# Performance work log

Measured on AMD Instinct MI355X. Metric: run time of the kernel, lower is better.

The kernel has to match this reference:

```python
import jax, jax.numpy as jnp
import numpy as np

TEMPERATURE = 0.1
B, T, D = 8, 1024, 1024
NEG_INF = -1e30

def setup_inputs() -> dict:
    key = jax.random.key(0)
    k1, k2, k3 = jax.random.split(key, 3)
    features = jax.random.normal(k1, (B, T, D), dtype=jnp.float32)
    masks = jax.random.bernoulli(k2, 0.05, (B, 1, T, T)).astype(jnp.float32)
    input_coords_length = jax.random.randint(k3, (B,), T // 2, T - 1)  # int32
    return {"features": features, "masks": masks, "input_coords_length": input_coords_length}


def _sup_con_loss(feat, mask, L):
    # feat: [T, D], mask: [T, T] float, L: scalar int valid length (slice [:L, :L])
    Tn = feat.shape[0]
    dt = feat.dtype
    vr = jnp.arange(Tn) < L                              # valid rows/cols [T]
    valid2d = (vr[:, None] & vr[None, :]).astype(dt)     # [T, T]
    dot = jnp.matmul(feat, feat.T) / TEMPERATURE         # [T, T]
    dot = jnp.where(vr[None, :], dot, NEG_INF)           # exclude padded cols from max
    logits = dot - jax.lax.stop_gradient(jnp.max(dot, axis=-1, keepdims=True))
    logits_mask = (1.0 - jnp.eye(Tn, dtype=dt)) * valid2d  # off-diagonal, in-slice
    exp_logits = jnp.exp(logits) * logits_mask
    m = mask * valid2d
    # negative_mask = 1-mask; entries < 1 zeroed (binary mask -> indicator of mask==0)
    neg = 1.0 - m
    neg = jnp.where(neg < 1.0, 0.0, neg) * valid2d
    # positive_mask = mask with entries > 0 set to 1
    pos = jnp.where(m > 0, 1.0, m)
    neg_denom = jnp.sum(exp_logits * neg, axis=-1, keepdims=True)
    pos_denom = jax.lax.stop_gradient(jnp.sum(exp_logits * pos, axis=-1, keepdims=True))
    log_prob = logits - jnp.log(neg_denom + pos_denom + 1e-6)
    m2 = m * logits_mask
    mean_log_prob_pos = (m2 * log_prob).sum(-1) / (m2.sum(-1) + 1e-6)  # [T]
    # mean over the L valid rows only (matches .mean() on the sliced tensor)
    return -jnp.sum(jnp.where(vr, mean_log_prob_pos, 0.0)) / L.astype(dt)


def _is_valid(mask, L):
    # valid sample iff sliced mask differs from eye(L) with [0,0]=0
    Tn = mask.shape[0]
    vr = jnp.arange(Tn) < L
    valid2d = (vr[:, None] & vr[None, :]).astype(mask.dtype)
    sanity = jnp.eye(Tn, dtype=mask.dtype).at[0, 0].set(0.0) * valid2d
    return jnp.any((mask * valid2d) != sanity)


def reference(features, masks, input_coords_length):
    L = input_coords_length + 1                      # [B]
    mask0 = masks[:, 0]                              # [B, T, T] (num_layers asserted == 1)
    losses = jax.vmap(_sup_con_loss)(features, mask0, L)   # [B]
    valid = jax.vmap(_is_valid)(mask0, L)                  # [B] bool
    vbs = jnp.maximum(jnp.sum(valid.astype(features.dtype)), 1.0)
    return jnp.sum(losses) / vbs
```

## Files before the change

kernel.cpp:

```cpp
#include <hip/hip_runtime.h>
#include <hip/hip_bf16.h>
#include <stdint.h>

#define T_DIM 1024
#define B_DIM 8

typedef __attribute__((ext_vector_type(8))) short short8;
typedef __attribute__((ext_vector_type(4))) float f32x4;

__device__ inline void gll16(const void* g, void* l) {
  __builtin_amdgcn_global_load_lds((__attribute__((address_space(1))) void*)g,
                                   (__attribute__((address_space(3))) void*)l,
                                   16, 0, 0);
}

__global__ __launch_bounds__(256) void convert_kernel(const float* __restrict__ F,
                                                      __hip_bfloat16* __restrict__ Fb) {
  const int t = blockIdx.x * 256 + threadIdx.x;
  const float4 v = ((const float4*)F)[t];
  union { __hip_bfloat16 h[4]; uint64_t u; } p;
  p.h[0] = __float2bfloat16(v.x);
  p.h[1] = __float2bfloat16(v.y);
  p.h[2] = __float2bfloat16(v.z);
  p.h[3] = __float2bfloat16(v.w);
  ((uint64_t*)Fb)[t] = p.u;
}

__global__ __launch_bounds__(256) void gram_kernel(const __hip_bfloat16* __restrict__ Fb,
                                                   float* __restrict__ S) {
  __shared__ __hip_bfloat16 As[128 * 32];
  __shared__ __hip_bfloat16 Bs[128 * 32];
  const int b = blockIdx.z;
  const __hip_bfloat16* F = Fb + ((size_t)b << 20);
  float* Sb = S + ((size_t)b << 20);
  const int tid  = threadIdx.x;
  const int lane = tid & 63;
  const int wave = tid >> 6;
  const int wrow = (wave >> 1) * 64;
  const int wcol = (wave & 1) * 64;
  const int row0 = blockIdx.y * 128;
  const int col0 = blockIdx.x * 128;

  const int sr = tid >> 2;
  const int sk = (tid & 3) * 8;

  f32x4 acc[4][4];
#pragma unroll
  for (int i = 0; i < 4; i++)
#pragma unroll
    for (int j = 0; j < 4; j++) acc[i][j] = (f32x4){0.f, 0.f, 0.f, 0.f};

  const int fr = lane & 15;
  const int fk = (lane >> 4) * 8;

  for (int k0 = 0; k0 < T_DIM; k0 += 32) {
    __syncthreads();
    gll16(F + (size_t)(row0 + sr) * T_DIM + k0 + sk,      As + tid * 8);
    gll16(F + (size_t)(row0 + sr + 64) * T_DIM + k0 + sk, As + 64 * 32 + tid * 8);
    gll16(F + (size_t)(col0 + sr) * T_DIM + k0 + sk,      Bs + tid * 8);
    gll16(F + (size_t)(col0 + sr + 64) * T_DIM + k0 + sk, Bs + 64 * 32 + tid * 8);
    __syncthreads();

    short8 af[4], bf[4];
#pragma unroll
    for (int t = 0; t < 4; t++) {
      af[t] = *(const short8*)(As + (wrow + t * 16 + fr) * 32 + fk);
      bf[t] = *(const short8*)(Bs + (wcol + t * 16 + fr) * 32 + fk);
    }
#pragma unroll
    for (int ti = 0; ti < 4; ti++)
#pragma unroll
      for (int tj = 0; tj < 4; tj++)
        acc[ti][tj] = __builtin_amdgcn_mfma_f32_16x16x32_bf16(af[ti], bf[tj], acc[ti][tj], 0, 0, 0);
  }

#pragma unroll
  for (int ti = 0; ti < 4; ti++)
#pragma unroll
    for (int tj = 0; tj < 4; tj++)
#pragma unroll
      for (int r = 0; r < 4; r++) {
        const int row = row0 + wrow + ti * 16 + (lane >> 4) * 4 + r;
        const int col = col0 + wcol + tj * 16 + (lane & 15);
        Sb[(size_t)row * T_DIM + col] = acc[ti][tj][r] * 10.0f;
      }
}

__global__ __launch_bounds__(256) void row_kernel(const float* __restrict__ S,
                                                  const float* __restrict__ M,
                                                  const int* __restrict__ icl,
                                                  float* __restrict__ row_val,
                                                  int* __restrict__ row_bad) {
  const int row = blockIdx.x;
  const int b = row >> 10;
  const int i = row & 1023;
  const int L = icl[b] + 1;
  if (i >= L) {
    if (threadIdx.x == 0) { row_val[row] = 0.0f; row_bad[row] = 0; }
    return;
  }
  const int tid  = threadIdx.x;
  const int lane = tid & 63;
  const int wave = tid >> 6;
  const float4 s4 = ((const float4*)(S + (size_t)row * T_DIM))[tid];
  const float4 m4 = ((const float4*)(M + (size_t)row * T_DIM))[tid];
  const float sv[4] = {s4.x, s4.y, s4.z, s4.w};
  const float mv[4] = {m4.x, m4.y, m4.z, m4.w};
  const int j0 = tid * 4;

  float mx = -1e30f;
#pragma unroll
  for (int c = 0; c < 4; c++)
    if (j0 + c < L) mx = fmaxf(mx, sv[c]);
  for (int o = 32; o > 0; o >>= 1) mx = fmaxf(mx, __shfl_down(mx, o, 64));
  __shared__ float wred[4];
  if (lane == 0) wred[wave] = mx;
  __syncthreads();
  mx = fmaxf(fmaxf(wred[0], wred[1]), fmaxf(wred[2], wred[3]));

  float den = 0.f, cnt = 0.f, asum = 0.f;
  bool bad = false;
#pragma unroll
  for (int c = 0; c < 4; c++) {
    const int j = j0 + c;
    if (j < L) {
      const float d = sv[c] - mx;
      const float mm = mv[c];
      if (j != i) {
        den += __expf(d);
        cnt += mm;
        asum += mm * d;
      }
      const float sane = (j == i && i != 0) ? 1.0f : 0.0f;
      bad = bad || (mm != sane);
    }
  }
  for (int o = 32; o > 0; o >>= 1) {
    den  += __shfl_down(den, o, 64);
    cnt  += __shfl_down(cnt, o, 64);
    asum += __shfl_down(asum, o, 64);
  }
  const bool wbad = (__ballot(bad) != 0ull);
  __shared__ float dred[4], cred[4], ared[4];
  __shared__ int bred[4];
  if (lane == 0) { dred[wave] = den; cred[wave] = cnt; ared[wave] = asum; bred[wave] = wbad ? 1 : 0; }
  __syncthreads();
  if (tid == 0) {
    const float D = dred[0] + dred[1] + dred[2] + dred[3];
    const float C = cred[0] + cred[1] + cred[2] + cred[3];
    const float A = ared[0] + ared[1] + ared[2] + ared[3];
    const float mlpp = (A - C * __logf(D + 1e-6f)) / (C + 1e-6f);
    row_val[row] = -mlpp / (float)L;
    row_bad[row] = bred[0] | bred[1] | bred[2] | bred[3];
  }
}

__global__ __launch_bounds__(256) void final_kernel(const float* __restrict__ row_val,
                                                    const int* __restrict__ row_bad,
                                                    float* __restrict__ out) {
  const int tid  = threadIdx.x;
  const int lane = tid & 63;
  const int wave = tid >> 6;
  __shared__ int vb[B_DIM];
  if (tid < B_DIM) vb[tid] = 0;
  __syncthreads();
  float lsum = 0.f;
  for (int idx = tid; idx < B_DIM * T_DIM; idx += 256) {
    lsum += row_val[idx];
    if (row_bad[idx]) atomicOr(&vb[idx >> 10], 1);
  }
  for (int o = 32; o > 0; o >>= 1) lsum += __shfl_down(lsum, o, 64);
  __shared__ float part[4];
  if (lane == 0) part[wave] = lsum;
  __syncthreads();
  if (tid == 0) {
    const float total = part[0] + part[1] + part[2] + part[3];
    int v = 0;
    for (int b = 0; b < B_DIM; b++) v += (vb[b] ? 1 : 0);
    out[0] = total / fmaxf((float)v, 1.0f);
  }
}

extern "C" void kernel_launch(void* const* d_in, const int* in_sizes, int n_in,
                              void* d_out, int out_size, void* d_ws, size_t ws_size,
                              hipStream_t stream) {
  const float* feat = (const float*)d_in[0];
  const float* mask = (const float*)d_in[1];
  const int*   icl  = (const int*)d_in[2];
  float* out = (float*)d_out;

  char* ws = (char*)d_ws;
  __hip_bfloat16* Fb = (__hip_bfloat16*)ws;
  float* S        = (float*)(ws + (16u << 20));
  float* row_val  = (float*)(ws + (48u << 20));
  int*   row_bad  = (int*)(ws + (48u << 20) + (32u << 10));

  convert_kernel<<<dim3(8192), dim3(256), 0, stream>>>(feat, Fb);
  gram_kernel<<<dim3(8, 8, 8), dim3(256), 0, stream>>>(Fb, S);
  row_kernel<<<dim3(8192), dim3(256), 0, stream>>>(S, mask, icl, row_val, row_bad);
  final_kernel<<<dim3(1), dim3(256), 0, stream>>>(row_val, row_bad, out);
}
```

Measured before the change: 144.0 us.

## Fuse Gram matmul with per-tile online softmax row statistics and skip padded tiles

Replaces the separate Gram-matrix write plus row-reduction kernel with a fused kernel. Each 128x128 tile computes the similarity block and immediately reduces it to per-row partial statistics (running max, exp-sum, masked sum, count, bad flag), merged by a small reduce kernel. This removes the 32MB fp32 S round trip. It also skips tiles entirely past the valid length, loads the operand once for diagonal tiles, and double-buffers 64-wide K stages. In exchange the kernel reads the mask with strided scalar loads in the epilogue and adds more shared memory and register pressure.

```diff
diff --git a/kernel.cpp b/kernel.cpp
--- a/kernel.cpp
+++ b/kernel.cpp
@@ -26,23 +26,36 @@
   ((uint64_t*)Fb)[t] = p.u;
 }
 
-__global__ __launch_bounds__(256) void gram_kernel(const __hip_bfloat16* __restrict__ Fb,
-                                                   float* __restrict__ S) {
-  __shared__ __hip_bfloat16 As[128 * 32];
-  __shared__ __hip_bfloat16 Bs[128 * 32];
-  const int b = blockIdx.z;
+__global__ __launch_bounds__(256) void fused_kernel(const __hip_bfloat16* __restrict__ Fb,
+                                                    const float* __restrict__ M,
+                                                    const int* __restrict__ icl,
+                                                    float* __restrict__ part) {
+  const int b  = blockIdx.z;
+  const int rt = blockIdx.y;
+  const int ct = blockIdx.x;
+  const int L  = icl[b] + 1;
+  if (rt * 128 >= L || ct * 128 >= L) return;
+
+  __shared__ __hip_bfloat16 As[2][8192];
+  __shared__ __hip_bfloat16 Bs[2][8192];
+  __shared__ float rp_m[128][2], rp_d[128][2], rp_s[128][2], rp_c[128][2], rp_b[128][2];
+
   const __hip_bfloat16* F = Fb + ((size_t)b << 20);
-  float* Sb = S + ((size_t)b << 20);
   const int tid  = threadIdx.x;
   const int lane = tid & 63;
   const int wave = tid >> 6;
   const int wrow = (wave >> 1) * 64;
   const int wcol = (wave & 1) * 64;
-  const int row0 = blockIdx.y * 128;
-  const int col0 = blockIdx.x * 128;
-
-  const int sr = tid >> 2;
-  const int sk = (tid & 3) * 8;
+  const int row0 = rt * 128;
+  const int col0 = ct * 128;
+  const bool diag = (rt == ct);
+
+  const int fr = lane & 15;
+  const int q  = lane >> 4;
+  const int fk = q * 8;
+
+  const int srow = tid >> 2;
+  const int skc  = (tid & 3) * 8;
 
   f32x4 acc[4][4];
 #pragma unroll
@@ -50,109 +63,125 @@
 #pragma unroll
     for (int j = 0; j < 4; j++) acc[i][j] = (f32x4){0.f, 0.f, 0.f, 0.f};
 
-  const int fr = lane & 15;
-  const int fk = (lane >> 4) * 8;
-
-  for (int k0 = 0; k0 < T_DIM; k0 += 32) {
+  auto stage = [&](int buf, int k0) {
+#pragma unroll
+    for (int p = 0; p < 4; p++) {
+      const int half = p & 1, kk = p >> 1;
+      gll16(F + (size_t)(row0 + half * 64 + srow) * T_DIM + k0 + kk * 32 + skc,
+            &As[buf][kk * 4096 + half * 2048 + tid * 8]);
+    }
+    if (!diag) {
+#pragma unroll
+      for (int p = 0; p < 4; p++) {
+        const int half = p & 1, kk = p >> 1;
+        gll16(F + (size_t)(col0 + half * 64 + srow) * T_DIM + k0 + kk * 32 + skc,
+              &Bs[buf][kk * 4096 + half * 2048 + tid * 8]);
+      }
+    }
+  };
+
+  stage(0, 0);
+  int cur = 0;
+  for (int ks = 0; ks < 16; ks++) {
     __syncthreads();
-    gll16(F + (size_t)(row0 + sr) * T_DIM + k0 + sk,      As + tid * 8);
-    gll16(F + (size_t)(row0 + sr + 64) * T_DIM + k0 + sk, As + 64 * 32 + tid * 8);
-    gll16(F + (size_t)(col0 + sr) * T_DIM + k0 + sk,      Bs + tid * 8);
-    gll16(F + (size_t)(col0 + sr + 64) * T_DIM + k0 + sk, Bs + 64 * 32 + tid * 8);
-    __syncthreads();
-
-    short8 af[4], bf[4];
-#pragma unroll
-    for (int t = 0; t < 4; t++) {
-      af[t] = *(const short8*)(As + (wrow + t * 16 + fr) * 32 + fk);
-      bf[t] = *(const short8*)(Bs + (wcol + t * 16 + fr) * 32 + fk);
-    }
-#pragma unroll
-    for (int ti = 0; ti < 4; ti++)
-#pragma unroll
-      for (int tj = 0; tj < 4; tj++)
-        acc[ti][tj] = __builtin_amdgcn_mfma_f32_16x16x32_bf16(af[ti], bf[tj], acc[ti][tj], 0, 0, 0);
-  }
-
-#pragma unroll
-  for (int ti = 0; ti < 4; ti++)
-#pragma unroll
-    for (int tj = 0; tj < 4; tj++)
-#pragma unroll
-      for (int r = 0; r < 4; r++) {
-        const int row = row0 + wrow + ti * 16 + (lane >> 4) * 4 + r;
-        const int col = col0 + wcol + tj * 16 + (lane & 15);
-        Sb[(size_t)row * T_DIM + col] = acc[ti][tj][r] * 10.0f;
-      }
-}
-
-__global__ __launch_bounds__(256) void row_kernel(const float* __restrict__ S,
-                                                  const float* __restrict__ M,
-                                                  const int* __restrict__ icl,
-                                                  float* __restrict__ row_val,
-                                                  int* __restrict__ row_bad) {
-  const int row = blockIdx.x;
+    if (ks + 1 < 16) stage(cur ^ 1, (ks + 1) * 64);
+#pragma unroll
+    for (int kk = 0; kk < 2; kk++) {
+      const __hip_bfloat16* Ab = &As[cur][kk * 4096];
+      const __hip_bfloat16* Bb = diag ? Ab : &Bs[cur][kk * 4096];
+      short8 af[4], bfr[4];
+#pragma unroll
+      for (int t = 0; t < 4; t++) {
+        af[t]  = *(const short8*)(Ab + (wrow + t * 16 + fr) * 32 + fk);
+        bfr[t] = *(const short8*)(Bb + (wcol + t * 16 + fr) * 32 + fk);
+      }
+#pragma unroll
+      for (int ti = 0; ti < 4; ti++)
+#pragma unroll
+        for (int tj = 0; tj < 4; tj++)
+          acc[ti][tj] = __builtin_amdgcn_mfma_f32_16x16x32_bf16(af[ti], bfr[tj], acc[ti][tj], 0, 0, 0);
+    }
+    cur ^= 1;
+  }
+
+  const float* Mb = M + ((size_t)b << 20);
+#pragma unroll
+  for (int ti = 0; ti < 4; ti++) {
+#pragma unroll
+    for (int r = 0; r < 4; r++) {
+      const int lrow = wrow + ti * 16 + q * 4 + r;
+      const int grow = row0 + lrow;
+      float m = -1e30f, den = 0.f, msum = 0.f, cnt = 0.f, badf = 0.f;
+#pragma unroll
+      for (int tj = 0; tj < 4; tj++) {
+        const int gcol = col0 + wcol + tj * 16 + fr;
+        if (gcol < L) {
+          const float s  = acc[ti][tj][r] * 10.0f;
+          const float mk = Mb[(size_t)grow * T_DIM + gcol];
+          const float nm = fmaxf(m, s);
+          const bool  dg = (gcol == grow);
+          den = den * __expf(m - nm) + (dg ? 0.f : __expf(s - nm));
+          m = nm;
+          if (!dg) { msum += mk * s; cnt += mk; }
+          const float sane = (dg && grow != 0) ? 1.f : 0.f;
+          badf = fmaxf(badf, (mk != sane) ? 1.f : 0.f);
+        }
+      }
+#pragma unroll
+      for (int d = 1; d < 16; d <<= 1) {
+        const float om  = __shfl_xor(m, d, 64);
+        const float od  = __shfl_xor(den, d, 64);
+        const float os  = __shfl_xor(msum, d, 64);
+        const float oc  = __shfl_xor(cnt, d, 64);
+        const float ob  = __shfl_xor(badf, d, 64);
+        const float nm  = fmaxf(m, om);
+        den = den * __expf(m - nm) + od * __expf(om - nm);
+        m = nm; msum += os; cnt += oc; badf = fmaxf(badf, ob);
+      }
+      if (fr == 0) {
+        const int h = wave & 1;
+        rp_m[lrow][h] = m;  rp_d[lrow][h] = den; rp_s[lrow][h] = msum;
+        rp_c[lrow][h] = cnt; rp_b[lrow][h] = badf;
+      }
+    }
+  }
+  __syncthreads();
+
+  if (tid < 128) {
+    const float m0 = rp_m[tid][0], m1 = rp_m[tid][1];
+    const float nm = fmaxf(m0, m1);
+    const float den = rp_d[tid][0] * __expf(m0 - nm) + rp_d[tid][1] * __expf(m1 - nm);
+    const float msum = rp_s[tid][0] + rp_s[tid][1];
+    const float cnt  = rp_c[tid][0] + rp_c[tid][1];
+    const float badf = fmaxf(rp_b[tid][0], rp_b[tid][1]);
+    float* p = part + ((((size_t)b * 1024 + row0 + tid) * 8) + ct) * 5;
+    p[0] = nm; p[1] = den; p[2] = msum; p[3] = cnt; p[4] = badf;
+  }
+}
+
+__global__ __launch_bounds__(256) void reduce_kernel(const float* __restrict__ part,
+                                                     const int* __restrict__ icl,
+                                                     float* __restrict__ row_val,
+                                                     int* __restrict__ row_bad) {
+  const int row = blockIdx.x * 256 + threadIdx.x;
   const int b = row >> 10;
   const int i = row & 1023;
   const int L = icl[b] + 1;
-  if (i >= L) {
-    if (threadIdx.x == 0) { row_val[row] = 0.0f; row_bad[row] = 0; }
-    return;
-  }
-  const int tid  = threadIdx.x;
-  const int lane = tid & 63;
-  const int wave = tid >> 6;
-  const float4 s4 = ((const float4*)(S + (size_t)row * T_DIM))[tid];
-  const float4 m4 = ((const float4*)(M + (size_t)row * T_DIM))[tid];
-  const float sv[4] = {s4.x, s4.y, s4.z, s4.w};
-  const float mv[4] = {m4.x, m4.y, m4.z, m4.w};
-  const int j0 = tid * 4;
-
-  float mx = -1e30f;
-#pragma unroll
-  for (int c = 0; c < 4; c++)
-    if (j0 + c < L) mx = fmaxf(mx, sv[c]);
-  for (int o = 32; o > 0; o >>= 1) mx = fmaxf(mx, __shfl_down(mx, o, 64));
-  __shared__ float wred[4];
-  if (lane == 0) wred[wave] = mx;
-  __syncthreads();
-  mx = fmaxf(fmaxf(wred[0], wred[1]), fmaxf(wred[2], wred[3]));
-
-  float den = 0.f, cnt = 0.f, asum = 0.f;
-  bool bad = false;
-#pragma unroll
-  for (int c = 0; c < 4; c++) {
-    const int j = j0 + c;
-    if (j < L) {
-      const float d = sv[c] - mx;
-      const float mm = mv[c];
-      if (j != i) {
-        den += __expf(d);
-        cnt += mm;
-        asum += mm * d;
-      }
-      const float sane = (j == i && i != 0) ? 1.0f : 0.0f;
-      bad = bad || (mm != sane);
-    }
-  }
-  for (int o = 32; o > 0; o >>= 1) {
-    den  += __shfl_down(den, o, 64);
-    cnt  += __shfl_down(cnt, o, 64);
-    asum += __shfl_down(asum, o, 64);
-  }
-  const bool wbad = (__ballot(bad) != 0ull);
-  __shared__ float dred[4], cred[4], ared[4];
-  __shared__ int bred[4];
-  if (lane == 0) { dred[wave] = den; cred[wave] = cnt; ared[wave] = asum; bred[wave] = wbad ? 1 : 0; }
-  __syncthreads();
-  if (tid == 0) {
-    const float D = dred[0] + dred[1] + dred[2] + dred[3];
-    const float C = cred[0] + cred[1] + cred[2] + cred[3];
-    const float A = ared[0] + ared[1] + ared[2] + ared[3];
-    const float mlpp = (A - C * __logf(D + 1e-6f)) / (C + 1e-6f);
-    row_val[row] = -mlpp / (float)L;
-    row_bad[row] = bred[0] | bred[1] | bred[2] | bred[3];
-  }
+  if (i >= L) { row_val[row] = 0.f; row_bad[row] = 0; return; }
+  const float* p = part + (size_t)row * 40;
+  const int ns = (L + 127) >> 7;
+  float m = -1e30f, den = 0.f, msum = 0.f, cnt = 0.f, badf = 0.f;
+  for (int s = 0; s < ns; s++) {
+    const float pm = p[s * 5 + 0], pd = p[s * 5 + 1];
+    const float nm = fmaxf(m, pm);
+    den = den * __expf(m - nm) + pd * __expf(pm - nm);
+    m = nm;
+    msum += p[s * 5 + 2]; cnt += p[s * 5 + 3]; badf = fmaxf(badf, p[s * 5 + 4]);
+  }
+  const float A = msum - cnt * m;
+  const float mlpp = (A - cnt * __logf(den + 1e-6f)) / (cnt + 1e-6f);
+  row_val[row] = -mlpp / (float)L;
+  row_bad[row] = badf > 0.f ? 1 : 0;
 }
 
 __global__ __launch_bounds__(256) void final_kernel(const float* __restrict__ row_val,
@@ -170,13 +199,13 @@
     if (row_bad[idx]) atomicOr(&vb[idx >> 10], 1);
   }
   for (int o = 32; o > 0; o >>= 1) lsum += __shfl_down(lsum, o, 64);
-  __shared__ float part[4];
-  if (lane == 0) part[wave] = lsum;
+  __shared__ float partl[4];
+  if (lane == 0) partl[wave] = lsum;
   __syncthreads();
   if (tid == 0) {
-    const float total = part[0] + part[1] + part[2] + part[3];
+    const float total = partl[0] + partl[1] + partl[2] + partl[3];
     int v = 0;
-    for (int b = 0; b < B_DIM; b++) v += (vb[b] ? 1 : 0);
+    for (int bb = 0; bb < B_DIM; bb++) v += (vb[bb] ? 1 : 0);
     out[0] = total / fmaxf((float)v, 1.0f);
   }
 }
@@ -191,12 +220,12 @@
 
   char* ws = (char*)d_ws;
   __hip_bfloat16* Fb = (__hip_bfloat16*)ws;
-  float* S        = (float*)(ws + (16u << 20));
-  float* row_val  = (float*)(ws + (48u << 20));
-  int*   row_bad  = (int*)(ws + (48u << 20) + (32u << 10));
+  float* part    = (float*)(ws + (16u << 20));
+  float* row_val = (float*)(ws + (18u << 20));
+  int*   row_bad = (int*)(ws + (18u << 20) + (32u << 10));
 
   convert_kernel<<<dim3(8192), dim3(256), 0, stream>>>(feat, Fb);
-  gram_kernel<<<dim3(8, 8, 8), dim3(256), 0, stream>>>(Fb, S);
-  row_kernel<<<dim3(8192), dim3(256), 0, stream>>>(S, mask, icl, row_val, row_bad);
+  fused_kernel<<<dim3(8, 8, 8), dim3(256), 0, stream>>>(Fb, mask, icl, part);
+  reduce_kernel<<<dim3(32), dim3(256), 0, stream>>>(part, icl, row_val, row_bad);
   final_kernel<<<dim3(1), dim3(256), 0, stream>>>(row_val, row_bad, out);
 }
```

New measurement: 154.4 us. 7.2% more time.
